# Kernel tuning notes

Hardware: AMD Instinct MI355X
Metric: run time of the kernel (lower is better)

## Reference

```python
import jax, jax.numpy as jnp
import numpy as np

N = 40000
E = 640000
D = 128
H = 128
NUM_LAYERS = 3


def _sage_conv(x, src, dst, Wl, Wr, b, num_nodes):
    # message: gather source-node features along each edge  [E, d]
    msg = x[src]
    # mean aggregation into destination nodes
    agg = jax.ops.segment_sum(msg, dst, num_segments=num_nodes)
    deg = jax.ops.segment_sum(jnp.ones((msg.shape[0],), dtype=x.dtype), dst,
                              num_segments=num_nodes)
    agg = agg / jnp.maximum(deg, 1.0)[:, None]
    # out = lin_l(agg) + lin_r(x); pyg lin_l carries the bias, lin_r has none
    return agg @ Wl + b + x @ Wr


def setup_inputs() -> dict:
    key = jax.random.key(0)
    ks = jax.random.split(key, 12)
    x = jax.random.normal(ks[0], (N, D), dtype=jnp.float32)
    edge_index = jax.random.randint(ks[1], (2, E), 0, N, dtype=jnp.int64)
    s = 1.0 / np.sqrt(D)
    inp = {"x": x, "edge_index": edge_index}
    for i in range(NUM_LAYERS):
        inp[f"Wl{i}"] = jax.random.normal(ks[2 + 3 * i], (D, H), dtype=jnp.float32) * s
        inp[f"Wr{i}"] = jax.random.normal(ks[3 + 3 * i], (D, H), dtype=jnp.float32) * s
        inp[f"b{i}"] = jnp.zeros((H,), dtype=jnp.float32)
    return inp


def reference(x, edge_index, Wl0, Wr0, b0, Wl1, Wr1, b1, Wl2, Wr2, b2):
    src, dst = edge_index[0], edge_index[1]
    params = [(Wl0, Wr0, b0), (Wl1, Wr1, b1), (Wl2, Wr2, b2)]
    h = x
    for i, (Wl, Wr, b) in enumerate(params):
        h = _sage_conv(h, src, dst, Wl, Wr, b, N)
        if i != NUM_LAYERS - 1:
            h = jax.nn.relu(h)
            # dropout p=0.5 is identity in eval mode (training=False)
    return h
```

## Files before the change

### kernel.cpp

```cpp
#include <hip/hip_runtime.h>
#include <hip/hip_bf16.h>

#define D 128
#define CAP 64

typedef __attribute__((ext_vector_type(4))) float f32x4;
typedef __attribute__((ext_vector_type(8))) short bf16x8;

static __device__ __forceinline__ unsigned short f2bf(float f) {
    union { float f; unsigned int u; } v; v.f = f;
    unsigned int r = v.u + 0x7fffu + ((v.u >> 16) & 1u);
    return (unsigned short)(r >> 16);
}
static __device__ __forceinline__ float bf2f_lo(unsigned int v) {
    union { unsigned int u; float f; } x; x.u = v << 16; return x.f;
}
static __device__ __forceinline__ float bf2f_hi(unsigned int v) {
    union { unsigned int u; float f; } x; x.u = v & 0xffff0000u; return x.f;
}

__global__ __launch_bounds__(256) void place_cvt_wt_kernel(
    const int* __restrict__ src, const int* __restrict__ dst,
    int* __restrict__ cnt, int* __restrict__ csr, int E_,
    const float* __restrict__ x, unsigned short* __restrict__ xb, int n4,
    const float* __restrict__ Wl0, const float* __restrict__ Wr0,
    const float* __restrict__ Wl1, const float* __restrict__ Wr1,
    const float* __restrict__ Wl2, const float* __restrict__ Wr2,
    unsigned short* __restrict__ WtB) {
    int bid = blockIdx.x;
    int nplace = (E_ + 255) >> 8;
    if (bid < nplace) {
        int e = bid * 256 + threadIdx.x;
        if (e < E_) {
            int d = dst[e];
            int pos = (d << 6) + atomicAdd(&cnt[d], 1);
            csr[pos] = src[e];
        }
        return;
    }
    bid -= nplace;
    int ncvt = (n4 + 255) >> 8;
    if (bid < ncvt) {
        int i = bid * 256 + threadIdx.x;
        if (i < n4) {
            float4 v = reinterpret_cast<const float4*>(x)[i];
            ushort4 o;
            o.x = f2bf(v.x); o.y = f2bf(v.y); o.z = f2bf(v.z); o.w = f2bf(v.w);
            reinterpret_cast<ushort4*>(xb)[i] = o;
        }
        return;
    }
    int idx = bid - ncvt;
    int layer = idx >> 4;
    int j = (idx & 15) * 256 + threadIdx.x;
    const float* Wl = (layer == 0) ? Wl0 : (layer == 1) ? Wl1 : Wl2;
    const float* Wr = (layer == 0) ? Wr0 : (layer == 1) ? Wr1 : Wr2;
    unsigned short* Wt = WtB + (size_t)layer * 128 * 256;
    int c = j >> 5;
    int g = j & 31;
    int k0 = g * 8;
    const float* Wsrc = (k0 < 128) ? (Wl + (size_t)k0 * D + c)
                                   : (Wr + (size_t)(k0 - 128) * D + c);
    float v[8];
#pragma unroll
    for (int i = 0; i < 8; ++i) v[i] = Wsrc[(size_t)i * D];
    uint4 o;
    o.x = (unsigned int)f2bf(v[0]) | ((unsigned int)f2bf(v[1]) << 16);
    o.y = (unsigned int)f2bf(v[2]) | ((unsigned int)f2bf(v[3]) << 16);
    o.z = (unsigned int)f2bf(v[4]) | ((unsigned int)f2bf(v[5]) << 16);
    o.w = (unsigned int)f2bf(v[6]) | ((unsigned int)f2bf(v[7]) << 16);
    *reinterpret_cast<uint4*>(Wt + (size_t)c * 256 + k0) = o;
}

__global__ __launch_bounds__(256) void gather_mean_bf16(
    const unsigned short* __restrict__ hb, const int* __restrict__ cnt,
    const int* __restrict__ csr, unsigned short* __restrict__ aggb, int N_) {
    int node = blockIdx.x * 4 + (threadIdx.x >> 6);
    int lane = threadIdx.x & 63;
    if (node >= N_) return;
    int beg = node << 6;
    int dgr = cnt[node];
    int end = beg + dgr;
    int q = lane >> 4;
    int t = lane & 15;

    const uint4* hb4 = reinterpret_cast<const uint4*>(hb);

    float acc[8];
#pragma unroll
    for (int i = 0; i < 8; ++i) acc[i] = 0.f;

#define ACC8(V)                                             \
    acc[0] += bf2f_lo(V.x); acc[1] += bf2f_hi(V.x);         \
    acc[2] += bf2f_lo(V.y); acc[3] += bf2f_hi(V.y);         \
    acc[4] += bf2f_lo(V.z); acc[5] += bf2f_hi(V.z);         \
    acc[6] += bf2f_lo(V.w); acc[7] += bf2f_hi(V.w);

    int e = beg + q;
    for (; e + 12 < end; e += 16) {
        int s0 = csr[e];
        int s1 = csr[e + 4];
        int s2 = csr[e + 8];
        int s3 = csr[e + 12];
        uint4 v0 = hb4[(size_t)s0 * 16 + t];
        uint4 v1 = hb4[(size_t)s1 * 16 + t];
        uint4 v2 = hb4[(size_t)s2 * 16 + t];
        uint4 v3 = hb4[(size_t)s3 * 16 + t];
        ACC8(v0); ACC8(v1); ACC8(v2); ACC8(v3);
    }
    for (; e < end; e += 4) {
        uint4 v0 = hb4[(size_t)csr[e] * 16 + t];
        ACC8(v0);
    }
#undef ACC8

#pragma unroll
    for (int i = 0; i < 8; ++i) {
        acc[i] += __shfl_xor(acc[i], 16, 64);
        acc[i] += __shfl_xor(acc[i], 32, 64);
    }
    if (q == 0) {
        float sc = 1.0f / (float)(dgr > 0 ? dgr : 1);
        uint4 o;
        o.x = (unsigned int)f2bf(acc[0] * sc) | ((unsigned int)f2bf(acc[1] * sc) << 16);
        o.y = (unsigned int)f2bf(acc[2] * sc) | ((unsigned int)f2bf(acc[3] * sc) << 16);
        o.z = (unsigned int)f2bf(acc[4] * sc) | ((unsigned int)f2bf(acc[5] * sc) << 16);
        o.w = (unsigned int)f2bf(acc[6] * sc) | ((unsigned int)f2bf(acc[7] * sc) << 16);
        reinterpret_cast<uint4*>(aggb + (size_t)node * D)[t] = o;
    }
}

template <int MODE>
__global__ __launch_bounds__(512) void sage_gemm_mfma(
    const unsigned short* __restrict__ hinb, const unsigned short* __restrict__ aggb,
    const unsigned short* __restrict__ WtB, const float* __restrict__ bias,
    void* __restrict__ out, int N_) {
    __shared__ unsigned short sWt[128][264];

    const int tid = threadIdx.x;
    for (int idx = tid; idx < 128 * 32; idx += 512) {
        int c = idx >> 5, g = idx & 31;
        *reinterpret_cast<uint4*>(&sWt[c][g * 8]) =
            reinterpret_cast<const uint4*>(WtB + (size_t)c * 256)[g];
    }
    __syncthreads();

    const int lane = tid & 63;
    const int w = tid >> 6;
    const int q = lane >> 4;
    const int c = lane & 15;
    const int R = blockIdx.x * 128 + w * 16;

    int r0 = R + c;  if (r0 > N_ - 1) r0 = N_ - 1;

    f32x4 acc[8];
#pragma unroll
    for (int n = 0; n < 8; ++n) acc[n] = (f32x4){0.f, 0.f, 0.f, 0.f};

#pragma unroll
    for (int ks = 0; ks < 8; ++ks) {
        int kg = ks * 32 + q * 8;
        const unsigned short* base = (kg < 128) ? (aggb + kg) : (hinb + (kg - 128));
        bf16x8 a0 = *reinterpret_cast<const bf16x8*>(base + (size_t)r0 * D);
#pragma unroll
        for (int n = 0; n < 8; ++n) {
            bf16x8 b = *reinterpret_cast<const bf16x8*>(&sWt[n * 16 + c][ks * 32 + q * 8]);
            acc[n] = __builtin_amdgcn_mfma_f32_16x16x32_bf16(a0, b, acc[n], 0, 0, 0);
        }
    }

    unsigned short* outb = (unsigned short*)out;
    float* outf = (float*)out;
#pragma unroll
    for (int n = 0; n < 8; ++n) {
        int col = n * 16 + c;
        float bv = bias[col];
#pragma unroll
        for (int r = 0; r < 4; ++r) {
            int row = R + q * 4 + r;
            if (row < N_) {
                float v = acc[n][r] + bv;
                if (MODE == 0) {
                    v = fmaxf(v, 0.f);
                    outb[(size_t)row * D + col] = f2bf(v);
                } else {
                    outf[(size_t)row * D + col] = v;
                }
            }
        }
    }
}

extern "C" void kernel_launch(void* const* d_in, const int* in_sizes, int n_in,
                              void* d_out, int out_size, void* d_ws, size_t ws_size,
                              hipStream_t stream) {
    const float* x = (const float*)d_in[0];
    const int* edge = (const int*)d_in[1];
    const float* Wl[3] = {(const float*)d_in[2], (const float*)d_in[5], (const float*)d_in[8]};
    const float* Wr[3] = {(const float*)d_in[3], (const float*)d_in[6], (const float*)d_in[9]};
    const float* bs[3] = {(const float*)d_in[4], (const float*)d_in[7], (const float*)d_in[10]};

    const int N_ = in_sizes[0] / D;
    const int E_ = in_sizes[1] / 2;
    const int* src = edge;
    const int* dst = edge + E_;

    char* ws = (char*)d_ws;
    size_t bmat = (size_t)N_ * D * sizeof(unsigned short);
    unsigned short* xb = (unsigned short*)ws;
    unsigned short* h1b = (unsigned short*)(ws + bmat);
    unsigned short* aggb = (unsigned short*)(ws + 2 * bmat);
    char* p = ws + 3 * bmat;
    int* cnt = (int*)p;         p += (size_t)N_ * 4;
    unsigned short* WtB = (unsigned short*)p; p += 3 * 128 * 256 * sizeof(unsigned short);
    int* csr = (int*)p;         p += (size_t)N_ * CAP * 4;

    const int ndeg = (E_ + 255) / 256;
    const int n4 = N_ * D / 4;
    const int ncvt = (n4 + 255) / 256;

    hipMemsetAsync(cnt, 0, (size_t)N_ * sizeof(int), stream);
    place_cvt_wt_kernel<<<ndeg + ncvt + 48, 256, 0, stream>>>(
        src, dst, cnt, csr, E_, x, xb, n4,
        Wl[0], Wr[0], Wl[1], Wr[1], Wl[2], Wr[2], WtB);

    int gemm_blocks = (N_ + 127) / 128;
    int gather_blocks = (N_ + 3) / 4;
    unsigned short* h2b = xb;

    gather_mean_bf16<<<gather_blocks, 256, 0, stream>>>(xb, cnt, csr, aggb, N_);
    sage_gemm_mfma<0><<<gemm_blocks, 512, 0, stream>>>(xb, aggb, WtB, bs[0], h1b, N_);
    gather_mean_bf16<<<gather_blocks, 256, 0, stream>>>(h1b, cnt, csr, aggb, N_);
    sage_gemm_mfma<0><<<gemm_blocks, 512, 0, stream>>>(h1b, aggb, WtB + 128 * 256, bs[1], h2b, N_);
    gather_mean_bf16<<<gather_blocks, 256, 0, stream>>>(h2b, cnt, csr, aggb, N_);
    sage_gemm_mfma<1><<<gemm_blocks, 512, 0, stream>>>(h2b, aggb, WtB + 2 * 128 * 256, bs[2], d_out, N_);
}
```

Measured before the change: 158.4 us.

## Store CSR neighbor indices as 16-bit and halve GEMM shared-memory weight tile

Neighbor indices in the bucketed CSR are stored as unsigned short instead of int, halving the index traffic in the placement and gather kernels. The GEMM kernel now loads all A fragments up front and stages the weight matrix into shared memory in two 128-column halves (aggregate part, then self part), halving LDS usage so more blocks can be resident. However N=40000 exceeds 65535? No, 40000 fits in 16 bits, but the encoding only works while node count stays below 65536, and the extra syncthreads/reload add some overhead.

```diff
diff --git a/kernel.cpp b/kernel.cpp
--- a/kernel.cpp
+++ b/kernel.cpp
@@ -21,7 +21,7 @@
 
 __global__ __launch_bounds__(256) void place_cvt_wt_kernel(
     const int* __restrict__ src, const int* __restrict__ dst,
-    int* __restrict__ cnt, int* __restrict__ csr, int E_,
+    int* __restrict__ cnt, unsigned short* __restrict__ csr, int E_,
     const float* __restrict__ x, unsigned short* __restrict__ xb, int n4,
     const float* __restrict__ Wl0, const float* __restrict__ Wr0,
     const float* __restrict__ Wl1, const float* __restrict__ Wr1,
@@ -34,7 +34,7 @@
         if (e < E_) {
             int d = dst[e];
             int pos = (d << 6) + atomicAdd(&cnt[d], 1);
-            csr[pos] = src[e];
+            csr[pos] = (unsigned short)src[e];
         }
         return;
     }
@@ -74,7 +74,8 @@
 
 __global__ __launch_bounds__(256) void gather_mean_bf16(
     const unsigned short* __restrict__ hb, const int* __restrict__ cnt,
-    const int* __restrict__ csr, unsigned short* __restrict__ aggb, int N_) {
+    const unsigned short* __restrict__ csr, unsigned short* __restrict__ aggb,
+    int N_) {
     int node = blockIdx.x * 4 + (threadIdx.x >> 6);
     int lane = threadIdx.x & 63;
     if (node >= N_) return;
@@ -135,39 +136,55 @@
     const unsigned short* __restrict__ hinb, const unsigned short* __restrict__ aggb,
     const unsigned short* __restrict__ WtB, const float* __restrict__ bias,
     void* __restrict__ out, int N_) {
-    __shared__ unsigned short sWt[128][264];
+    __shared__ unsigned short sWt[128][136];
 
     const int tid = threadIdx.x;
-    for (int idx = tid; idx < 128 * 32; idx += 512) {
-        int c = idx >> 5, g = idx & 31;
-        *reinterpret_cast<uint4*>(&sWt[c][g * 8]) =
-            reinterpret_cast<const uint4*>(WtB + (size_t)c * 256)[g];
-    }
-    __syncthreads();
-
     const int lane = tid & 63;
     const int w = tid >> 6;
     const int q = lane >> 4;
     const int c = lane & 15;
     const int R = blockIdx.x * 128 + w * 16;
-
     int r0 = R + c;  if (r0 > N_ - 1) r0 = N_ - 1;
 
+    bf16x8 a_agg[4], a_hin[4];
+#pragma unroll
+    for (int ks = 0; ks < 4; ++ks) {
+        a_agg[ks] = *reinterpret_cast<const bf16x8*>(aggb + (size_t)r0 * D + ks * 32 + q * 8);
+        a_hin[ks] = *reinterpret_cast<const bf16x8*>(hinb + (size_t)r0 * D + ks * 32 + q * 8);
+    }
+
     f32x4 acc[8];
 #pragma unroll
     for (int n = 0; n < 8; ++n) acc[n] = (f32x4){0.f, 0.f, 0.f, 0.f};
 
-#pragma unroll
-    for (int ks = 0; ks < 8; ++ks) {
-        int kg = ks * 32 + q * 8;
-        const unsigned short* base = (kg < 128) ? (aggb + kg) : (hinb + (kg - 128));
-        bf16x8 a0 = *reinterpret_cast<const bf16x8*>(base + (size_t)r0 * D);
+    for (int idx = tid; idx < 128 * 16; idx += 512) {
+        int cc = idx >> 4, g = idx & 15;
+        *reinterpret_cast<uint4*>(&sWt[cc][g * 8]) =
+            *reinterpret_cast<const uint4*>(WtB + (size_t)cc * 256 + g * 8);
+    }
+    __syncthreads();
+#pragma unroll
+    for (int ks = 0; ks < 4; ++ks)
 #pragma unroll
         for (int n = 0; n < 8; ++n) {
             bf16x8 b = *reinterpret_cast<const bf16x8*>(&sWt[n * 16 + c][ks * 32 + q * 8]);
-            acc[n] = __builtin_amdgcn_mfma_f32_16x16x32_bf16(a0, b, acc[n], 0, 0, 0);
-        }
-    }
+            acc[n] = __builtin_amdgcn_mfma_f32_16x16x32_bf16(a_agg[ks], b, acc[n], 0, 0, 0);
+        }
+    __syncthreads();
+
+    for (int idx = tid; idx < 128 * 16; idx += 512) {
+        int cc = idx >> 4, g = idx & 15;
+        *reinterpret_cast<uint4*>(&sWt[cc][g * 8]) =
+            *reinterpret_cast<const uint4*>(WtB + (size_t)cc * 256 + 128 + g * 8);
+    }
+    __syncthreads();
+#pragma unroll
+    for (int ks = 0; ks < 4; ++ks)
+#pragma unroll
+        for (int n = 0; n < 8; ++n) {
+            bf16x8 b = *reinterpret_cast<const bf16x8*>(&sWt[n * 16 + c][ks * 32 + q * 8]);
+            acc[n] = __builtin_amdgcn_mfma_f32_16x16x32_bf16(a_hin[ks], b, acc[n], 0, 0, 0);
+        }
 
     unsigned short* outb = (unsigned short*)out;
     float* outf = (float*)out;
@@ -213,14 +230,14 @@
     char* p = ws + 3 * bmat;
     int* cnt = (int*)p;         p += (size_t)N_ * 4;
     unsigned short* WtB = (unsigned short*)p; p += 3 * 128 * 256 * sizeof(unsigned short);
-    int* csr = (int*)p;         p += (size_t)N_ * CAP * 4;
-
-    const int ndeg = (E_ + 255) / 256;
+    unsigned short* csr = (unsigned short*)p; p += (size_t)N_ * CAP * 2;
+
+    const int nplace = (E_ + 255) / 256;
     const int n4 = N_ * D / 4;
     const int ncvt = (n4 + 255) / 256;
 
     hipMemsetAsync(cnt, 0, (size_t)N_ * sizeof(int), stream);
-    place_cvt_wt_kernel<<<ndeg + ncvt + 48, 256, 0, stream>>>(
+    place_cvt_wt_kernel<<<nplace + ncvt + 48, 256, 0, stream>>>(
         src, dst, cnt, csr, E_, x, xb, n4,
         Wl[0], Wr[0], Wl[1], Wr[1], Wl[2], Wr[2], WtB);
 
```

New measurement: 167.4 us. +5.7%, slower.
